# Kernel tuning notes

Measured on AMD Instinct MI355X. Metric: run time of the kernel, lower is better.

Reference implementation:

```python
import jax, jax.numpy as jnp
import numpy as np

B, T, E = 128, 128, 1024
MD = 50          # mask_dim
H = 256          # per-direction GRU hidden (l_hidden_size=512)
D = 512          # biGRU output dim
CO = 256         # conv output channels
K = 4            # CRF tags (2+2)
NL = 3           # sentiment labels
C1, C2 = 0.1, 0.1


def setup_inputs() -> dict:
    key = jax.random.key(0)
    ks = jax.random.split(key, 16)
    IN = E + MD
    g = lambda k, s, sc=0.05: jax.random.normal(k, s, dtype=jnp.float32) * sc
    z = lambda s: jnp.zeros(s, jnp.float32)
    return {
        "sents": jax.random.normal(ks[0], (B, T, E), dtype=jnp.float32),
        "masks": jax.random.randint(ks[1], (B, T), 0, 2),
        "labels": jax.random.randint(ks[2], (B,), 0, NL),
        "lens": jnp.maximum(jax.random.randint(ks[3], (B,), 1, T + 1), 1),
        "mask_emb": g(ks[4], (2, MD), 1.0),
        "Wih_f": g(ks[5], (3 * H, IN)), "Whh_f": g(ks[6], (3 * H, H)),
        "bih_f": z((3 * H,)), "bhh_f": z((3 * H,)),
        "Wih_b": g(ks[7], (3 * H, IN)), "Whh_b": g(ks[8], (3 * H, H)),
        "bih_b": z((3 * H,)), "bhh_b": z((3 * H,)),
        "conv_w": g(ks[9], (CO, D, 3)), "conv_b": z((CO,)),
        "W_tri": g(ks[10], (K, CO)), "b_tri": z((K,)),
        "transitions": g(ks[11], (K, K), 1.0),
        "W_lab": g(ks[12], (NL, CO)), "b_lab": z((NL,)),
    }


def _gru(xg, mask, Whh, bhh, reverse):
    # xg: [T,B,3H] precomputed input projections; mask: [T,B,1]
    Hh = Whh.shape[1]

    def step(h, inp):
        gg, m = inp
        hg = h @ Whh.T + bhh
        r = jax.nn.sigmoid(gg[:, :Hh] + hg[:, :Hh])
        zt = jax.nn.sigmoid(gg[:, Hh:2 * Hh] + hg[:, Hh:2 * Hh])
        n = jnp.tanh(gg[:, 2 * Hh:] + r * hg[:, 2 * Hh:])
        hn = (1.0 - zt) * n + zt * h
        hn = m * hn + (1.0 - m) * h  # padded steps carry state (packed-seq semantics)
        return hn, hn

    h0 = jnp.zeros((xg.shape[1], Hh), xg.dtype)
    _, hs = jax.lax.scan(step, h0, (xg, mask), reverse=reverse)
    return hs  # [T,B,H]


def reference(sents, masks, labels, lens, mask_emb, Wih_f, Whh_f, bih_f, bhh_f,
              Wih_b, Whh_b, bih_b, bhh_b, conv_w, conv_b, W_tri, b_tri,
              transitions, W_lab, b_lab):
    wm = (jnp.arange(T)[None, :] < lens[:, None]).astype(jnp.float32)  # [B,T]
    # SimpleCatTgtMasked: concat mask embedding
    x = jnp.concatenate([sents, mask_emb[masks]], axis=-1)  # [B,T,E+MD]
    mT = wm.T[:, :, None]  # [T,B,1]
    xg_f = jnp.einsum('btc,gc->tbg', x, Wih_f) + bih_f
    xg_b = jnp.einsum('btc,gc->tbg', x, Wih_b) + bih_b
    hf = _gru(xg_f, mT, Whh_f, bhh_f, False)
    hb = _gru(xg_b, mT, Whh_b, bhh_b, True)
    ctx = jnp.concatenate([hf, hb], axis=-1).transpose(1, 0, 2)  # [B,T,D]
    # Conv1d(D->CO, k=3, pad=1) + ReLU
    c = jax.lax.conv_general_dilated(ctx.transpose(0, 2, 1), conv_w, (1,), ((1, 1),),
                                     dimension_numbers=('NCH', 'OIH', 'NCH'))
    ctx2 = jax.nn.relu(c + conv_b[None, :, None]).transpose(0, 2, 1)  # [B,T,CO]
    feats = jnp.einsum('btc,kc->btk', ctx2, W_tri) + b_tri  # [B,T,K]
    # masked linear-chain CRF forward-backward (log-space)
    fT = feats.transpose(1, 0, 2)  # [T,B,K]
    mS = wm.T[1:, :, None]         # [T-1,B,1]

    def fstep(a, inp):
        f_t, m_t = inp
        an = f_t + jax.nn.logsumexp(a[:, :, None] + transitions[None], axis=1)
        a = m_t * an + (1.0 - m_t) * a
        return a, a

    a0 = fT[0]
    _, alphas = jax.lax.scan(fstep, a0, (fT[1:], mS))
    alpha = jnp.concatenate([a0[None], alphas], axis=0)  # [T,B,K]

    def bstep(b, inp):
        f_n, m_n = inp  # feats/mask at t+1
        bn = jax.nn.logsumexp(transitions[None] + (f_n + b)[:, None, :], axis=2)
        b = m_n * bn + (1.0 - m_n) * b
        return b, b

    b_last = jnp.zeros_like(a0)
    _, betas = jax.lax.scan(bstep, b_last, (fT[1:], mS), reverse=True)
    beta = jnp.concatenate([betas, b_last[None]], axis=0)  # [T,B,K]

    marg = jax.nn.softmax(alpha + beta, axis=-1)  # [T,B,K], = exp(alpha+beta-logZ)
    sp = marg[:, :, 1].T * wm  # [B,T] select polarity, zero past length
    gamma = sp.sum(axis=1) / 2.0
    sent_v = jnp.einsum('bt,btc->bc', sp, ctx2) / gamma[:, None]  # [B,CO]
    scores = sent_v @ W_lab.T + b_lab  # [B,NL]
    logp = jax.nn.log_softmax(scores, axis=1)
    cls_loss = -jnp.mean(logp[jnp.arange(B), labels])
    pena = jax.nn.relu(transitions[1, 0] - transitions[0, 0]) + \
           jax.nn.relu(transitions[0, 1] - transitions[1, 1])
    s_prob_norm = jnp.mean(sp.sum(axis=1))
    norm_pen = C1 * pena + C2 * s_prob_norm
    return jnp.stack([cls_loss, norm_pen])
```

## Files before the change

kernel.cpp:

```cpp
#include <hip/hip_runtime.h>
#include <hip/hip_bf16.h>
#include <math.h>

#define B_ 128
#define T_ 128
#define E_ 1024
#define IN_ 1074
#define H_ 256
#define G3_ 768
#define D_ 512
#define CO_ 256

typedef unsigned int uint_t;
typedef _Float16 v2h __attribute__((ext_vector_type(2)));
typedef _Float16 f16x8 __attribute__((ext_vector_type(8)));
typedef float f32x4 __attribute__((ext_vector_type(4)));


__global__ void k_prep_me(const float* __restrict__ mask_emb,
                          const float* __restrict__ Wf, const float* __restrict__ bf,
                          const float* __restrict__ Wb, const float* __restrict__ bb,
                          float* __restrict__ me) {
    int idx = blockIdx.x * 256 + threadIdx.x;
    if (idx >= 2 * 2 * G3_) return;
    int dir = idx / (2 * G3_);
    int rem = idx % (2 * G3_);
    int m = rem / G3_;
    int g = rem % G3_;
    const float* W = dir ? Wb : Wf;
    const float* bi = dir ? bb : bf;
    float acc = bi[g];
    const float* wrow = W + (size_t)g * IN_ + E_;
    const float* e = mask_emb + m * 50;
    #pragma unroll 10
    for (int c = 0; c < 50; ++c) acc += e[c] * wrow[c];
    me[idx] = acc;
}

__device__ __forceinline__ uint_t pk2(float a, float b) {
    uint_t u0 = (uint_t)__builtin_bit_cast(unsigned short, (_Float16)a);
    uint_t u1 = (uint_t)__builtin_bit_cast(unsigned short, (_Float16)b);
    return u0 | (u1 << 16);
}

__global__ void k_prep_wh(const float* __restrict__ Wf, const float* __restrict__ Wb,
                          uint_t* __restrict__ wq) {
    int idx = blockIdx.x * 256 + threadIdx.x;
    if (idx >= 196608) return;
    int u = idx & 3;
    int j = (idx >> 2) & 255;
    int rest = idx >> 10;
    int p = rest % 3;
    int dq = rest / 3;
    int q = dq & 31;
    int d = dq >> 5;
    int g = p * 256 + j;
    int kp = 4 * q + u;
    const float* W = d ? Wb : Wf;
    float w0 = W[(size_t)g * H_ + 2 * kp];
    float w1 = W[(size_t)g * H_ + 2 * kp + 1];
    wq[idx] = pk2(w0, w1);
}

__global__ void k_prep_w2(const float* __restrict__ cw, unsigned short* __restrict__ W2) {
    int i = blockIdx.x * 256 + threadIdx.x;
    if (i >= CO_ * 1536) return;
    int co = i / 1536;
    int k = i % 1536;
    int j = k >> 9;
    int d = k & 511;
    float v = cw[(size_t)co * (D_ * 3) + d * 3 + j];
    W2[i] = __builtin_bit_cast(unsigned short, (_Float16)v);
}

__global__ __launch_bounds__(256) void k_cvt_sents(const float* __restrict__ in,
                                                   uint_t* __restrict__ out) {
    int i = blockIdx.x * 256 + threadIdx.x;
    float4 a = reinterpret_cast<const float4*>(in)[i * 2];
    float4 b = reinterpret_cast<const float4*>(in)[i * 2 + 1];
    uint4 o;
    o.x = pk2(a.x, a.y); o.y = pk2(a.z, a.w);
    o.z = pk2(b.x, b.y); o.w = pk2(b.z, b.w);
    reinterpret_cast<uint4*>(out)[i] = o;
}

__global__ __launch_bounds__(256) void k_cvt_w(const float* __restrict__ Wf,
                                               const float* __restrict__ Wb,
                                               uint_t* __restrict__ out) {
    int i = blockIdx.x * 256 + threadIdx.x;
    if (i >= 1536 * 128) return;
    int n = i >> 7, kq = i & 127;
    int dir = n >= G3_;
    int g = n - dir * G3_;
    const float* src = (dir ? Wb : Wf) + (size_t)g * IN_ + kq * 8;
    float2 a = reinterpret_cast<const float2*>(src)[0];
    float2 b = reinterpret_cast<const float2*>(src)[1];
    float2 c = reinterpret_cast<const float2*>(src)[2];
    float2 d = reinterpret_cast<const float2*>(src)[3];
    uint4 o;
    o.x = pk2(a.x, a.y); o.y = pk2(b.x, b.y);
    o.z = pk2(c.x, c.y); o.w = pk2(d.x, d.y);
    reinterpret_cast<uint4*>(out)[i] = o;
}


__device__ __forceinline__ void gload16(const void* g, void* l) {
    __builtin_amdgcn_global_load_lds(
        (const __attribute__((address_space(1))) void*)g,
        (__attribute__((address_space(3))) void*)l, 16, 0, 0);
}

__global__ __launch_bounds__(256) void k_gemm_mfma(
        const _Float16* __restrict__ A16, const _Float16* __restrict__ W16,
        const float* __restrict__ me, const int* __restrict__ masks,
        float* __restrict__ xgf, float* __restrict__ xgb) {
    __shared__ _Float16 As[4096];
    __shared__ _Float16 Bs[4096];
    const int bid = blockIdx.x;
    const int logical = (bid & 7) * 192 + (bid >> 3);
    const int mt = logical / 12, nt = logical % 12;
    const int bm = mt * 128, bn = nt * 128;
    const int tid = threadIdx.x;
    const int w = tid >> 6, lane = tid & 63;
    const int wr = w >> 1, wc = w & 1;

    const int rl = lane & 15;
    const int kb = (lane >> 4) * 16;
    const int st0 = w, st1 = 4 + w;
    const char* gA0 = (const char*)A16 + (size_t)(bm + st0 * 16 + rl) * 2048 + kb;
    const char* gA1 = (const char*)A16 + (size_t)(bm + st1 * 16 + rl) * 2048 + kb;
    const char* gB0 = (const char*)W16 + (size_t)(bn + st0 * 16 + rl) * 2048 + kb;
    const char* gB1 = (const char*)W16 + (size_t)(bn + st1 * 16 + rl) * 2048 + kb;
    char* lA0 = (char*)As + w * 1024;
    char* lA1 = (char*)As + 4096 + w * 1024;
    char* lB0 = (char*)Bs + w * 1024;
    char* lB1 = (char*)Bs + 4096 + w * 1024;

    f32x4 acc[4][4];
    #pragma unroll
    for (int m = 0; m < 4; ++m)
        #pragma unroll
        for (int n = 0; n < 4; ++n)
            acc[m][n] = (f32x4){0.f, 0.f, 0.f, 0.f};

    for (int kB = 0; kB < 2048; kB += 64) {
        gload16(gA0 + kB, lA0);
        gload16(gA1 + kB, lA1);
        gload16(gB0 + kB, lB0);
        gload16(gB1 + kB, lB1);
        __syncthreads();
        f16x8 af[4], bf[4];
        #pragma unroll
        for (int m = 0; m < 4; ++m)
            af[m] = *reinterpret_cast<const f16x8*>(
                (const char*)As + (wr * 4 + m) * 1024 + lane * 16);
        #pragma unroll
        for (int n = 0; n < 4; ++n)
            bf[n] = *reinterpret_cast<const f16x8*>(
                (const char*)Bs + (wc * 4 + n) * 1024 + lane * 16);
        #pragma unroll
        for (int m = 0; m < 4; ++m)
            #pragma unroll
            for (int n = 0; n < 4; ++n)
                acc[m][n] = __builtin_amdgcn_mfma_f32_16x16x32_f16(
                    af[m], bf[n], acc[m][n], 0, 0, 0);
        __syncthreads();
    }

    const int qr = (lane >> 4) * 4;
    const int cc = lane & 15;
    #pragma unroll
    for (int m = 0; m < 4; ++m) {
        #pragma unroll
        for (int q = 0; q < 4; ++q) {
            const int bt = bm + wr * 64 + m * 16 + qr + q;
            const int mk = masks[bt];
            const int b = bt >> 7, t = bt & 127;
            #pragma unroll
            for (int n = 0; n < 4; ++n) {
                const int col = bn + wc * 64 + n * 16 + cc;
                const int dir = col >= G3_;
                const int g = col - dir * G3_;
                float v = acc[m][n][q] + me[dir * (2 * G3_) + mk * G3_ + g];
                float* dst = (dir ? xgb : xgf) + ((size_t)(t * B_ + b)) * G3_ + g;
                *dst = v;
            }
        }
    }
}

__device__ __forceinline__ float dot2(uint_t w, uint_t h, float acc) {
#if __has_builtin(__builtin_amdgcn_fdot2)
    return __builtin_amdgcn_fdot2(__builtin_bit_cast(v2h, w),
                                  __builtin_bit_cast(v2h, h), acc, false);
#else
    v2h a = __builtin_bit_cast(v2h, w), b = __builtin_bit_cast(v2h, h);
    return acc + (float)a[0] * (float)b[0] + (float)a[1] * (float)b[1];
#endif
}

__global__ __launch_bounds__(512, 2) void k_gru(
        const float* __restrict__ xgf, const float* __restrict__ xgb,
        const uint_t* __restrict__ wq,
        const float* __restrict__ bhhf, const float* __restrict__ bhhb,
        const int* __restrict__ lens, _Float16* __restrict__ ctx16p) {
    const int dir = blockIdx.y;
    const int b = blockIdx.x;
    const int tid = threadIdx.x;
    const int j = tid & 255;
    const int half = tid >> 8;
    const float* xg = dir ? xgb : xgf;
    const float* bhh = dir ? bhhb : bhhf;
    const uint4* wq4 = (const uint4*)wq + (size_t)dir * (32 * 3 * 256);
    _Float16* c16 = ctx16p + (size_t)b * (T_ + 2) * D_;

    __shared__ uint4 hs4[32];
    __shared__ float part[3][256];
    _Float16* hsf = (_Float16*)hs4;

    c16[tid] = (_Float16)0.f;
    c16[(size_t)(T_ + 1) * D_ + tid] = (_Float16)0.f;

    uint4 w4[3][16];
    #pragma unroll
    for (int c = 0; c < 16; ++c) {
        const int q = half * 16 + c;
        #pragma unroll
        for (int p = 0; p < 3; ++p)
            w4[p][c] = wq4[((size_t)q * 3 + p) * 256 + j];
    }

    if (tid < 32) hs4[tid] = (uint4){0u, 0u, 0u, 0u};
    const int len = lens[b];
    const float bh0 = bhh[j], bh1 = bhh[H_ + j], bh2 = bhh[2 * H_ + j];
    float hcur = 0.f;
    float g0 = 0.f, g1 = 0.f, g2 = 0.f;
    int t = dir ? (T_ - 1) : 0;
    if (half == 0) {
        const float* r = xg + ((size_t)(t * B_ + b)) * G3_;
        g0 = r[j]; g1 = r[H_ + j]; g2 = r[2 * H_ + j];
    }
    __syncthreads();

    for (int s = 0; s < T_; ++s) {
        const int tn = dir ? (T_ - 2 - s) : (s + 1);
        float n0 = 0.f, n1 = 0.f, n2 = 0.f;
        if (half == 0 && s < T_ - 1) {
            const float* r = xg + ((size_t)(tn * B_ + b)) * G3_;
            n0 = r[j]; n1 = r[H_ + j]; n2 = r[2 * H_ + j];
        }
        float a0 = 0.f, a1 = 0.f, a2 = 0.f;
        #pragma unroll
        for (int c = 0; c < 16; ++c) {
            uint4 hp = hs4[half * 16 + c];
            a0 = dot2(w4[0][c].x, hp.x, a0); a0 = dot2(w4[0][c].y, hp.y, a0);
            a0 = dot2(w4[0][c].z, hp.z, a0); a0 = dot2(w4[0][c].w, hp.w, a0);
            a1 = dot2(w4[1][c].x, hp.x, a1); a1 = dot2(w4[1][c].y, hp.y, a1);
            a1 = dot2(w4[1][c].z, hp.z, a1); a1 = dot2(w4[1][c].w, hp.w, a1);
            a2 = dot2(w4[2][c].x, hp.x, a2); a2 = dot2(w4[2][c].y, hp.y, a2);
            a2 = dot2(w4[2][c].z, hp.z, a2); a2 = dot2(w4[2][c].w, hp.w, a2);
        }
        if (half == 1) {
            part[0][j] = a0; part[1][j] = a1; part[2][j] = a2;
        }
        __syncthreads();
        if (half == 0) {
            a0 += part[0][j]; a1 += part[1][j]; a2 += part[2][j];
            float rg = 1.f / (1.f + expf(-(g0 + a0 + bh0)));
            float zg = 1.f / (1.f + expf(-(g1 + a1 + bh1)));
            float ng = tanhf(g2 + rg * (a2 + bh2));
            float v = (1.f - zg) * ng + zg * hcur;
            hcur = (t < len) ? v : hcur;
            _Float16 h16 = (_Float16)hcur;
            c16[(size_t)(t + 1) * D_ + dir * H_ + j] = h16;
            hsf[j] = h16;
        }
        __syncthreads();
        g0 = n0; g1 = n1; g2 = n2;
        t = tn;
    }
}

__global__ __launch_bounds__(256) void k_conv_mfma(
        const _Float16* __restrict__ C16, const _Float16* __restrict__ W2,
        const float* __restrict__ cb, float* __restrict__ ctx2) {
    __shared__ _Float16 As[4096];
    __shared__ _Float16 Bs[4096];
    const int b = blockIdx.x >> 1;
    const int nt = blockIdx.x & 1;
    const int bn = nt * 128;
    const int tid = threadIdx.x;
    const int w = tid >> 6, lane = tid & 63;
    const int wr = w >> 1, wc = w & 1;
    const int rl = lane & 15;
    const int kb = (lane >> 4) * 16;
    const char* gA0 = (const char*)C16 + ((size_t)(b * (T_ + 2) + w * 16 + rl)) * 1024 + kb;
    const char* gA1 = (const char*)C16 + ((size_t)(b * (T_ + 2) + 64 + w * 16 + rl)) * 1024 + kb;
    const char* gB0 = (const char*)W2 + (size_t)(bn + w * 16 + rl) * 3072 + kb;
    const char* gB1 = (const char*)W2 + (size_t)(bn + 64 + w * 16 + rl) * 3072 + kb;
    char* lA0 = (char*)As + w * 1024;
    char* lA1 = (char*)As + 4096 + w * 1024;
    char* lB0 = (char*)Bs + w * 1024;
    char* lB1 = (char*)Bs + 4096 + w * 1024;

    f32x4 acc[4][4];
    #pragma unroll
    for (int m = 0; m < 4; ++m)
        #pragma unroll
        for (int n = 0; n < 4; ++n)
            acc[m][n] = (f32x4){0.f, 0.f, 0.f, 0.f};

    for (int kB = 0; kB < 3072; kB += 64) {
        gload16(gA0 + kB, lA0);
        gload16(gA1 + kB, lA1);
        gload16(gB0 + kB, lB0);
        gload16(gB1 + kB, lB1);
        __syncthreads();
        f16x8 af[4], bf[4];
        #pragma unroll
        for (int m = 0; m < 4; ++m)
            af[m] = *reinterpret_cast<const f16x8*>(
                (const char*)As + (wr * 4 + m) * 1024 + lane * 16);
        #pragma unroll
        for (int n = 0; n < 4; ++n)
            bf[n] = *reinterpret_cast<const f16x8*>(
                (const char*)Bs + (wc * 4 + n) * 1024 + lane * 16);
        #pragma unroll
        for (int m = 0; m < 4; ++m)
            #pragma unroll
            for (int n = 0; n < 4; ++n)
                acc[m][n] = __builtin_amdgcn_mfma_f32_16x16x32_f16(
                    af[m], bf[n], acc[m][n], 0, 0, 0);
        __syncthreads();
    }

    const int qr = (lane >> 4) * 4;
    const int cc = lane & 15;
    #pragma unroll
    for (int m = 0; m < 4; ++m) {
        #pragma unroll
        for (int q = 0; q < 4; ++q) {
            const int t = wr * 64 + m * 16 + qr + q;
            #pragma unroll
            for (int n = 0; n < 4; ++n) {
                const int co = bn + wc * 64 + n * 16 + cc;
                float v = acc[m][n][q] + cb[co];
                ctx2[((size_t)(b * T_ + t)) * CO_ + co] = fmaxf(v, 0.f);
            }
        }
    }
}

__global__ __launch_bounds__(256) void k_head(
        const float* __restrict__ ctx2, const float* __restrict__ W_tri,
        const float* __restrict__ b_tri, const float* __restrict__ trans,
        const float* __restrict__ W_lab, const float* __restrict__ b_lab,
        const int* __restrict__ lens, const int* __restrict__ labels,
        float* __restrict__ loss_b, float* __restrict__ spsum_b) {
    const int b = blockIdx.x;
    const int tid = threadIdx.x;
    const int w = tid >> 6, lane = tid & 63;
    __shared__ float f_s[T_][4];
    __shared__ float al[T_][4];
    __shared__ float be[T_][4];
    __shared__ float sp_s[T_];
    __shared__ float sv_s[CO_];
    __shared__ float sred[4];
    __shared__ float s_spsum;
    const int len = lens[b];
    const float* base = ctx2 + (size_t)b * T_ * CO_;

    {
        float wt[4][4];
        #pragma unroll
        for (int k = 0; k < 4; ++k)
            #pragma unroll
            for (int q = 0; q < 4; ++q)
                wt[k][q] = W_tri[k * CO_ + lane + 64 * q];
        float bt0 = b_tri[0], bt1 = b_tri[1], bt2 = b_tri[2], bt3 = b_tri[3];
        for (int t = w; t < T_; t += 4) {
            const float* row = base + (size_t)t * CO_;
            float v0 = row[lane], v1 = row[lane + 64],
                  v2 = row[lane + 128], v3 = row[lane + 192];
            float p0 = v0 * wt[0][0] + v1 * wt[0][1] + v2 * wt[0][2] + v3 * wt[0][3];
            float p1 = v0 * wt[1][0] + v1 * wt[1][1] + v2 * wt[1][2] + v3 * wt[1][3];
            float p2 = v0 * wt[2][0] + v1 * wt[2][1] + v2 * wt[2][2] + v3 * wt[2][3];
            float p3 = v0 * wt[3][0] + v1 * wt[3][1] + v2 * wt[3][2] + v3 * wt[3][3];
            #pragma unroll
            for (int off = 32; off > 0; off >>= 1) {
                p0 += __shfl_xor(p0, off);
                p1 += __shfl_xor(p1, off);
                p2 += __shfl_xor(p2, off);
                p3 += __shfl_xor(p3, off);
            }
            if (lane == 0) {
                f_s[t][0] = p0 + bt0; f_s[t][1] = p1 + bt1;
                f_s[t][2] = p2 + bt2; f_s[t][3] = p3 + bt3;
            }
        }
    }
    __syncthreads();

    if (w == 0 && lane < 4) {
        const int j = lane;
        float tc0 = trans[0 * 4 + j], tc1 = trans[1 * 4 + j],
              tc2 = trans[2 * 4 + j], tc3 = trans[3 * 4 + j];
        float a = f_s[0][j];
        al[0][j] = a;
        for (int t = 1; t < T_; ++t) {
            float a0 = __shfl(a, 0), a1 = __shfl(a, 1),
                  a2 = __shfl(a, 2), a3 = __shfl(a, 3);
            float s0 = a0 + tc0, s1 = a1 + tc1, s2 = a2 + tc2, s3 = a3 + tc3;
            float m = fmaxf(fmaxf(s0, s1), fmaxf(s2, s3));
            float sum = expf(s0 - m) + expf(s1 - m) + expf(s2 - m) + expf(s3 - m);
            float an = f_s[t][j] + m + logf(sum);
            if (t < len) a = an;
            al[t][j] = a;
        }
    } else if (w == 1 && lane < 4) {
        const int i = lane;
        float tr0 = trans[i * 4 + 0], tr1 = trans[i * 4 + 1],
              tr2 = trans[i * 4 + 2], tr3 = trans[i * 4 + 3];
        float bb = 0.f;
        be[T_ - 1][i] = 0.f;
        for (int t = T_ - 2; t >= 0; --t) {
            float b0 = __shfl(bb, 0), b1 = __shfl(bb, 1),
                  b2 = __shfl(bb, 2), b3 = __shfl(bb, 3);
            float s0 = tr0 + f_s[t + 1][0] + b0;
            float s1 = tr1 + f_s[t + 1][1] + b1;
            float s2 = tr2 + f_s[t + 1][2] + b2;
            float s3 = tr3 + f_s[t + 1][3] + b3;
            float m = fmaxf(fmaxf(s0, s1), fmaxf(s2, s3));
            float sum = expf(s0 - m) + expf(s1 - m) + expf(s2 - m) + expf(s3 - m);
            float bn = m + logf(sum);
            if (t + 1 < len) bb = bn;
            be[t][i] = bb;
        }
    }
    __syncthreads();

    if (tid < T_) {
        int t = tid;
        float s0 = al[t][0] + be[t][0];
        float s1 = al[t][1] + be[t][1];
        float s2 = al[t][2] + be[t][2];
        float s3 = al[t][3] + be[t][3];
        float m = fmaxf(fmaxf(s0, s1), fmaxf(s2, s3));
        float e0 = expf(s0 - m), e1 = expf(s1 - m), e2 = expf(s2 - m), e3 = expf(s3 - m);
        float p1 = e1 / (e0 + e1 + e2 + e3);
        sp_s[t] = (t < len) ? p1 : 0.f;
    }
    __syncthreads();
    if (w == 0) {
        float s = sp_s[lane] + sp_s[lane + 64];
        #pragma unroll
        for (int off = 32; off > 0; off >>= 1) s += __shfl_xor(s, off);
        if (lane == 0) s_spsum = s;
    }
    __syncthreads();
    const float spsum = s_spsum;

    {
        float acc0 = 0.f, acc1 = 0.f, acc2 = 0.f, acc3 = 0.f;
        #pragma unroll 2
        for (int t = 0; t < T_; t += 4) {
            acc0 += sp_s[t + 0] * base[(size_t)(t + 0) * CO_ + tid];
            acc1 += sp_s[t + 1] * base[(size_t)(t + 1) * CO_ + tid];
            acc2 += sp_s[t + 2] * base[(size_t)(t + 2) * CO_ + tid];
            acc3 += sp_s[t + 3] * base[(size_t)(t + 3) * CO_ + tid];
        }
        sv_s[tid] = (acc0 + acc1 + acc2 + acc3) * 2.f / spsum;
    }
    __syncthreads();

    if (w < 3) {
        const float* wl = W_lab + w * CO_;
        float p = sv_s[lane] * wl[lane] + sv_s[lane + 64] * wl[lane + 64]
                + sv_s[lane + 128] * wl[lane + 128] + sv_s[lane + 192] * wl[lane + 192];
        #pragma unroll
        for (int off = 32; off > 0; off >>= 1) p += __shfl_xor(p, off);
        if (lane == 0) sred[w] = p + b_lab[w];
    }
    __syncthreads();
    if (tid == 0) {
        float m = fmaxf(sred[0], fmaxf(sred[1], sred[2]));
        float lse = m + logf(expf(sred[0] - m) + expf(sred[1] - m) + expf(sred[2] - m));
        loss_b[b] = lse - sred[labels[b]];
        spsum_b[b] = spsum;
    }
}

__global__ void k_final(const float* __restrict__ loss_b, const float* __restrict__ spsum_b,
                        const float* __restrict__ trans, float* __restrict__ out) {
    __shared__ float s1[128], s2[128];
    int tid = threadIdx.x;
    s1[tid] = loss_b[tid];
    s2[tid] = spsum_b[tid];
    __syncthreads();
    for (int off = 64; off > 0; off >>= 1) {
        if (tid < off) { s1[tid] += s1[tid + off]; s2[tid] += s2[tid + off]; }
        __syncthreads();
    }
    if (tid == 0) {
        float pena = fmaxf(trans[1 * 4 + 0] - trans[0 * 4 + 0], 0.f)
                   + fmaxf(trans[0 * 4 + 1] - trans[1 * 4 + 1], 0.f);
        out[0] = s1[0] / (float)B_;
        out[1] = 0.1f * pena + 0.1f * (s2[0] / (float)B_);
    }
}

extern "C" void kernel_launch(void* const* d_in, const int* in_sizes, int n_in,
                              void* d_out, int out_size, void* d_ws, size_t ws_size,
                              hipStream_t stream) {
    const float* sents   = (const float*)d_in[0];
    const int*   masks   = (const int*)d_in[1];
    const int*   labels  = (const int*)d_in[2];
    const int*   lens    = (const int*)d_in[3];
    const float* mask_emb= (const float*)d_in[4];
    const float* Wih_f   = (const float*)d_in[5];
    const float* Whh_f   = (const float*)d_in[6];
    const float* bih_f   = (const float*)d_in[7];
    const float* bhh_f   = (const float*)d_in[8];
    const float* Wih_b   = (const float*)d_in[9];
    const float* Whh_b   = (const float*)d_in[10];
    const float* bih_b   = (const float*)d_in[11];
    const float* bhh_b   = (const float*)d_in[12];
    const float* conv_w  = (const float*)d_in[13];
    const float* conv_b  = (const float*)d_in[14];
    const float* W_tri   = (const float*)d_in[15];
    const float* b_tri   = (const float*)d_in[16];
    const float* trans   = (const float*)d_in[17];
    const float* W_lab   = (const float*)d_in[18];
    const float* b_lab   = (const float*)d_in[19];
    float* out = (float*)d_out;
    float* ws = (float*)d_ws;

    const size_t o_xgf  = 0;
    const size_t o_xgb  = o_xgf  + (size_t)B_ * T_ * G3_;
    const size_t o_ctx  = o_xgb  + (size_t)B_ * T_ * G3_;
    const size_t o_ctx2 = o_ctx  + (size_t)B_ * T_ * D_;
    const size_t o_wp   = o_ctx2 + (size_t)B_ * T_ * CO_;
    const size_t o_me   = o_wp   + (size_t)2 * 32 * 3 * 256 * 4;
    const size_t o_w2   = o_me   + 2 * 2 * G3_;
    const size_t o_lossb= o_w2   + (size_t)D_ * 3 * CO_;
    const size_t o_spsum= o_lossb + B_;

    float* xgf  = ws + o_xgf;
    float* xgb  = ws + o_xgb;
    float* ctx  = ws + o_ctx;
    float* ctx2 = ws + o_ctx2;
    uint_t* wq  = (uint_t*)(ws + o_wp);
    float* me   = ws + o_me;
    unsigned short* W2 = (unsigned short*)(ws + o_w2);
    float* lossb = ws + o_lossb;
    float* spsumb = ws + o_spsum;

    _Float16* sents16 = (_Float16*)ctx;
    _Float16* ctx16p = (_Float16*)ctx;
    _Float16* W16 = (_Float16*)ctx2;

    k_prep_me<<<12, 256, 0, stream>>>(mask_emb, Wih_f, bih_f, Wih_b, bih_b, me);
    k_prep_wh<<<768, 256, 0, stream>>>(Whh_f, Whh_b, wq);
    k_prep_w2<<<1536, 256, 0, stream>>>(conv_w, W2);
    k_cvt_sents<<<8192, 256, 0, stream>>>(sents, (uint_t*)sents16);
    k_cvt_w<<<768, 256, 0, stream>>>(Wih_f, Wih_b, (uint_t*)W16);
    k_gemm_mfma<<<1536, 256, 0, stream>>>(sents16, W16, me, masks, xgf, xgb);
    k_gru<<<dim3(B_, 2), 512, 0, stream>>>(xgf, xgb, wq, bhh_f, bhh_b, lens, ctx16p);
    k_conv_mfma<<<256, 256, 0, stream>>>(ctx16p, (const _Float16*)W2, conv_b, ctx2);
    k_head<<<128, 256, 0, stream>>>(ctx2, W_tri, b_tri, trans, W_lab, b_lab,
                                    lens, labels, lossb, spsumb);
    k_final<<<1, 128, 0, stream>>>(lossb, spsumb, trans, out);
}
```

Baseline: 418.3 us.

## Split GRU recurrent matvec by gate across three thread groups

The GRU recurrence kernel moves from 512 threads, each splitting the hidden dimension in halves across all three gates, to 768 threads where each 256-thread group computes one full gate over the whole hidden vector. This removes the per-thread three-gate accumulation chains, shortens the per-step dependency chain of dot products, and keeps 32 uint4 weight registers per thread pinned with an empty asm. It costs more threads per block, and with launch bounds of 768 threads and 3 blocks per unit it risks register pressure or spilling. The combine step now reads two partial gates from shared memory instead of three.

```diff
diff --git a/kernel.cpp b/kernel.cpp
--- a/kernel.cpp
+++ b/kernel.cpp
@@ -199,7 +199,7 @@
 #endif
 }
 
-__global__ __launch_bounds__(512, 2) void k_gru(
+__global__ __launch_bounds__(768, 3) void k_gru(
         const float* __restrict__ xgf, const float* __restrict__ xgb,
         const uint_t* __restrict__ wq,
         const float* __restrict__ bhhf, const float* __restrict__ bhhb,
@@ -208,35 +208,38 @@
     const int b = blockIdx.x;
     const int tid = threadIdx.x;
     const int j = tid & 255;
-    const int half = tid >> 8;
+    const int p = tid >> 8;
     const float* xg = dir ? xgb : xgf;
     const float* bhh = dir ? bhhb : bhhf;
     const uint4* wq4 = (const uint4*)wq + (size_t)dir * (32 * 3 * 256);
     _Float16* c16 = ctx16p + (size_t)b * (T_ + 2) * D_;
 
     __shared__ uint4 hs4[32];
-    __shared__ float part[3][256];
+    __shared__ float part[2][256];
     _Float16* hsf = (_Float16*)hs4;
 
-    c16[tid] = (_Float16)0.f;
-    c16[(size_t)(T_ + 1) * D_ + tid] = (_Float16)0.f;
-
-    uint4 w4[3][16];
+    if (tid < 512) {
+        c16[tid] = (_Float16)0.f;
+        c16[(size_t)(T_ + 1) * D_ + tid] = (_Float16)0.f;
+    }
+
+    uint4 w4[32];
     #pragma unroll
-    for (int c = 0; c < 16; ++c) {
-        const int q = half * 16 + c;
-        #pragma unroll
-        for (int p = 0; p < 3; ++p)
-            w4[p][c] = wq4[((size_t)q * 3 + p) * 256 + j];
-    }
+    for (int c = 0; c < 32; ++c)
+        w4[c] = wq4[((size_t)c * 3 + p) * 256 + j];
+    #pragma unroll
+    for (int c = 0; c < 32; ++c)
+        asm volatile("" : "+v"(w4[c].x), "+v"(w4[c].y),
+                          "+v"(w4[c].z), "+v"(w4[c].w));
 
     if (tid < 32) hs4[tid] = (uint4){0u, 0u, 0u, 0u};
     const int len = lens[b];
-    const float bh0 = bhh[j], bh1 = bhh[H_ + j], bh2 = bhh[2 * H_ + j];
+    const float bh = bhh[p * H_ + j];
+    const float bh2o = bhh[2 * H_ + j];
     float hcur = 0.f;
     float g0 = 0.f, g1 = 0.f, g2 = 0.f;
     int t = dir ? (T_ - 1) : 0;
-    if (half == 0) {
+    if (p == 0) {
         const float* r = xg + ((size_t)(t * B_ + b)) * G3_;
         g0 = r[j]; g1 = r[H_ + j]; g2 = r[2 * H_ + j];
     }
@@ -245,30 +248,26 @@
     for (int s = 0; s < T_; ++s) {
         const int tn = dir ? (T_ - 2 - s) : (s + 1);
         float n0 = 0.f, n1 = 0.f, n2 = 0.f;
-        if (half == 0 && s < T_ - 1) {
+        if (p == 0 && s < T_ - 1) {
             const float* r = xg + ((size_t)(tn * B_ + b)) * G3_;
             n0 = r[j]; n1 = r[H_ + j]; n2 = r[2 * H_ + j];
         }
-        float a0 = 0.f, a1 = 0.f, a2 = 0.f;
-        #pragma unroll
-        for (int c = 0; c < 16; ++c) {
-            uint4 hp = hs4[half * 16 + c];
-            a0 = dot2(w4[0][c].x, hp.x, a0); a0 = dot2(w4[0][c].y, hp.y, a0);
-            a0 = dot2(w4[0][c].z, hp.z, a0); a0 = dot2(w4[0][c].w, hp.w, a0);
-            a1 = dot2(w4[1][c].x, hp.x, a1); a1 = dot2(w4[1][c].y, hp.y, a1);
-            a1 = dot2(w4[1][c].z, hp.z, a1); a1 = dot2(w4[1][c].w, hp.w, a1);
-            a2 = dot2(w4[2][c].x, hp.x, a2); a2 = dot2(w4[2][c].y, hp.y, a2);
-            a2 = dot2(w4[2][c].z, hp.z, a2); a2 = dot2(w4[2][c].w, hp.w, a2);
-        }
-        if (half == 1) {
-            part[0][j] = a0; part[1][j] = a1; part[2][j] = a2;
-        }
-        __syncthreads();
-        if (half == 0) {
-            a0 += part[0][j]; a1 += part[1][j]; a2 += part[2][j];
-            float rg = 1.f / (1.f + expf(-(g0 + a0 + bh0)));
-            float zg = 1.f / (1.f + expf(-(g1 + a1 + bh1)));
-            float ng = tanhf(g2 + rg * (a2 + bh2));
+        float a = 0.f;
+        #pragma unroll
+        for (int c = 0; c < 32; ++c) {
+            uint4 hp = hs4[c];
+            a = dot2(w4[c].x, hp.x, a);
+            a = dot2(w4[c].y, hp.y, a);
+            a = dot2(w4[c].z, hp.z, a);
+            a = dot2(w4[c].w, hp.w, a);
+        }
+        if (p > 0) part[p - 1][j] = a;
+        __syncthreads();
+        if (p == 0) {
+            float a0 = a, a1 = part[0][j], a2 = part[1][j];
+            float rg = 1.f / (1.f + expf(-(g0 + a0 + bh)));
+            float zg = 1.f / (1.f + expf(-(g1 + a1 + bhh[H_ + j])));
+            float ng = tanhf(g2 + rg * (a2 + bh2o));
             float v = (1.f - zg) * ng + zg * hcur;
             hcur = (t < len) ? v : hcur;
             _Float16 h16 = (_Float16)hcur;
@@ -565,7 +564,7 @@
     k_cvt_sents<<<8192, 256, 0, stream>>>(sents, (uint_t*)sents16);
     k_cvt_w<<<768, 256, 0, stream>>>(Wih_f, Wih_b, (uint_t*)W16);
     k_gemm_mfma<<<1536, 256, 0, stream>>>(sents16, W16, me, masks, xgf, xgb);
-    k_gru<<<dim3(B_, 2), 512, 0, stream>>>(xgf, xgb, wq, bhh_f, bhh_b, lens, ctx16p);
+    k_gru<<<dim3(B_, 2), 768, 0, stream>>>(xgf, xgb, wq, bhh_f, bhh_b, lens, ctx16p);
     k_conv_mfma<<<256, 256, 0, stream>>>(ctx16p, (const _Float16*)W2, conv_b, ctx2);
     k_head<<<128, 256, 0, stream>>>(ctx2, W_tri, b_tri, trans, W_lab, b_lab,
                                     lens, labels, lossb, spsumb);
```

After: 439.0 us. 1.05x slower.

## Quantize GRU recurrent weights and hidden state to int8 with sdot4

Applied to the files above, without the earlier changes.

Replaces the fp16 fdot2 recurrent matvec in the GRU with int8 per-row-scaled weights and an int8-quantized hidden state (scale 127), accumulated in integers via sdot4 and dequantized before the gates. Two new prep kernels compute per-row max-abs scales and pack the weights. The aim is to halve weight register footprint and dot-product instruction count in the serial recurrence, at the cost of much coarser numerical precision in the recurrent path, which may break accuracy tolerance.

```diff
diff --git a/kernel.cpp b/kernel.cpp
--- a/kernel.cpp
+++ b/kernel.cpp
@@ -43,23 +43,44 @@
     return u0 | (u1 << 16);
 }
 
-__global__ void k_prep_wh(const float* __restrict__ Wf, const float* __restrict__ Wb,
-                          uint_t* __restrict__ wq) {
-    int idx = blockIdx.x * 256 + threadIdx.x;
-    if (idx >= 196608) return;
-    int u = idx & 3;
-    int j = (idx >> 2) & 255;
-    int rest = idx >> 10;
+__global__ void k_scale(const float* __restrict__ Wf, const float* __restrict__ Wb,
+                        float* __restrict__ dq, float* __restrict__ inv) {
+    int r = blockIdx.x * 256 + threadIdx.x;
+    if (r >= 1536) return;
+    int d = r / G3_;
+    int g = r % G3_;
+    const float* W = (d ? Wb : Wf) + (size_t)g * H_;
+    float m = 0.f;
+    for (int k = 0; k < H_; ++k) m = fmaxf(m, fabsf(W[k]));
+    dq[r] = m / 16129.f;
+    inv[r] = (m > 0.f) ? 127.f / m : 0.f;
+}
+
+__global__ void k_quant(const float* __restrict__ Wf, const float* __restrict__ Wb,
+                        const float* __restrict__ inv, uint_t* __restrict__ wi8) {
+    int i = blockIdx.x * 256 + threadIdx.x;
+    if (i >= 98304) return;
+    int w = i & 3;
+    int j = (i >> 2) & 255;
+    int rest = i >> 10;
     int p = rest % 3;
-    int dq = rest / 3;
-    int q = dq & 31;
-    int d = dq >> 5;
+    int rest2 = rest / 3;
+    int q16 = rest2 & 7;
+    int khd = rest2 >> 3;
+    int kh = khd & 1;
+    int d = khd >> 1;
     int g = p * 256 + j;
-    int kp = 4 * q + u;
-    const float* W = d ? Wb : Wf;
-    float w0 = W[(size_t)g * H_ + 2 * kp];
-    float w1 = W[(size_t)g * H_ + 2 * kp + 1];
-    wq[idx] = pk2(w0, w1);
+    int k0 = kh * 128 + q16 * 16 + w * 4;
+    const float* W = (d ? Wb : Wf) + (size_t)g * H_ + k0;
+    float iv = inv[d * G3_ + g];
+    uint_t u = 0;
+    #pragma unroll
+    for (int c = 0; c < 4; ++c) {
+        int q = __float2int_rn(W[c] * iv);
+        q = max(-127, min(127, q));
+        u |= ((uint_t)(q & 0xff)) << (8 * c);
+    }
+    wi8[i] = u;
 }
 
 __global__ void k_prep_w2(const float* __restrict__ cw, unsigned short* __restrict__ W2) {
@@ -189,54 +210,57 @@
     }
 }
 
-__device__ __forceinline__ float dot2(uint_t w, uint_t h, float acc) {
-#if __has_builtin(__builtin_amdgcn_fdot2)
-    return __builtin_amdgcn_fdot2(__builtin_bit_cast(v2h, w),
-                                  __builtin_bit_cast(v2h, h), acc, false);
+__device__ __forceinline__ int sdot4(uint_t a, uint_t b, int c) {
+#if __has_builtin(__builtin_amdgcn_sdot4)
+    return __builtin_amdgcn_sdot4((int)a, (int)b, c, false);
 #else
-    v2h a = __builtin_bit_cast(v2h, w), b = __builtin_bit_cast(v2h, h);
-    return acc + (float)a[0] * (float)b[0] + (float)a[1] * (float)b[1];
+    int r = c;
+    r += ((int)(a << 24) >> 24) * ((int)(b << 24) >> 24);
+    r += ((int)(a << 16) >> 24) * ((int)(b << 16) >> 24);
+    r += ((int)(a << 8) >> 24) * ((int)(b << 8) >> 24);
+    r += ((int)a >> 24) * ((int)b >> 24);
+    return r;
 #endif
 }
 
 __global__ __launch_bounds__(512, 2) void k_gru(
         const float* __restrict__ xgf, const float* __restrict__ xgb,
-        const uint_t* __restrict__ wq,
+        const uint_t* __restrict__ wi8, const float* __restrict__ dq,
         const float* __restrict__ bhhf, const float* __restrict__ bhhb,
         const int* __restrict__ lens, _Float16* __restrict__ ctx16p) {
     const int dir = blockIdx.y;
     const int b = blockIdx.x;
     const int tid = threadIdx.x;
     const int j = tid & 255;
-    const int half = tid >> 8;
+    const int kh = tid >> 8;
     const float* xg = dir ? xgb : xgf;
     const float* bhh = dir ? bhhb : bhhf;
-    const uint4* wq4 = (const uint4*)wq + (size_t)dir * (32 * 3 * 256);
+    const uint4* wp4 = (const uint4*)wi8 + (size_t)dir * (2 * 8 * 3 * 256);
     _Float16* c16 = ctx16p + (size_t)b * (T_ + 2) * D_;
 
-    __shared__ uint4 hs4[32];
-    __shared__ float part[3][256];
-    _Float16* hsf = (_Float16*)hs4;
+    __shared__ uint_t hq_s[64];
+    __shared__ int part[3][256];
 
     c16[tid] = (_Float16)0.f;
     c16[(size_t)(T_ + 1) * D_ + tid] = (_Float16)0.f;
 
-    uint4 w4[3][16];
+    uint4 w4[3][8];
     #pragma unroll
-    for (int c = 0; c < 16; ++c) {
-        const int q = half * 16 + c;
+    for (int q = 0; q < 8; ++q)
         #pragma unroll
         for (int p = 0; p < 3; ++p)
-            w4[p][c] = wq4[((size_t)q * 3 + p) * 256 + j];
-    }
-
-    if (tid < 32) hs4[tid] = (uint4){0u, 0u, 0u, 0u};
+            w4[p][q] = wp4[((size_t)((kh * 8 + q) * 3 + p)) * 256 + j];
+
+    if (tid < 64) hq_s[tid] = 0u;
     const int len = lens[b];
+    const float dq0 = dq[dir * G3_ + j];
+    const float dq1 = dq[dir * G3_ + 256 + j];
+    const float dq2 = dq[dir * G3_ + 512 + j];
     const float bh0 = bhh[j], bh1 = bhh[H_ + j], bh2 = bhh[2 * H_ + j];
     float hcur = 0.f;
     float g0 = 0.f, g1 = 0.f, g2 = 0.f;
     int t = dir ? (T_ - 1) : 0;
-    if (half == 0) {
+    if (kh == 0) {
         const float* r = xg + ((size_t)(t * B_ + b)) * G3_;
         g0 = r[j]; g1 = r[H_ + j]; g2 = r[2 * H_ + j];
     }
@@ -245,35 +269,38 @@
     for (int s = 0; s < T_; ++s) {
         const int tn = dir ? (T_ - 2 - s) : (s + 1);
         float n0 = 0.f, n1 = 0.f, n2 = 0.f;
-        if (half == 0 && s < T_ - 1) {
+        if (kh == 0 && s < T_ - 1) {
             const float* r = xg + ((size_t)(tn * B_ + b)) * G3_;
             n0 = r[j]; n1 = r[H_ + j]; n2 = r[2 * H_ + j];
         }
-        float a0 = 0.f, a1 = 0.f, a2 = 0.f;
-        #pragma unroll
-        for (int c = 0; c < 16; ++c) {
-            uint4 hp = hs4[half * 16 + c];
-            a0 = dot2(w4[0][c].x, hp.x, a0); a0 = dot2(w4[0][c].y, hp.y, a0);
-            a0 = dot2(w4[0][c].z, hp.z, a0); a0 = dot2(w4[0][c].w, hp.w, a0);
-            a1 = dot2(w4[1][c].x, hp.x, a1); a1 = dot2(w4[1][c].y, hp.y, a1);
-            a1 = dot2(w4[1][c].z, hp.z, a1); a1 = dot2(w4[1][c].w, hp.w, a1);
-            a2 = dot2(w4[2][c].x, hp.x, a2); a2 = dot2(w4[2][c].y, hp.y, a2);
-            a2 = dot2(w4[2][c].z, hp.z, a2); a2 = dot2(w4[2][c].w, hp.w, a2);
-        }
-        if (half == 1) {
+        int a0 = 0, a1 = 0, a2 = 0;
+        const uint4* hv = (const uint4*)hq_s + kh * 8;
+        #pragma unroll
+        for (int q = 0; q < 8; ++q) {
+            uint4 h4 = hv[q];
+            a0 = sdot4(w4[0][q].x, h4.x, a0); a0 = sdot4(w4[0][q].y, h4.y, a0);
+            a0 = sdot4(w4[0][q].z, h4.z, a0); a0 = sdot4(w4[0][q].w, h4.w, a0);
+            a1 = sdot4(w4[1][q].x, h4.x, a1); a1 = sdot4(w4[1][q].y, h4.y, a1);
+            a1 = sdot4(w4[1][q].z, h4.z, a1); a1 = sdot4(w4[1][q].w, h4.w, a1);
+            a2 = sdot4(w4[2][q].x, h4.x, a2); a2 = sdot4(w4[2][q].y, h4.y, a2);
+            a2 = sdot4(w4[2][q].z, h4.z, a2); a2 = sdot4(w4[2][q].w, h4.w, a2);
+        }
+        if (kh == 1) {
             part[0][j] = a0; part[1][j] = a1; part[2][j] = a2;
         }
         __syncthreads();
-        if (half == 0) {
-            a0 += part[0][j]; a1 += part[1][j]; a2 += part[2][j];
-            float rg = 1.f / (1.f + expf(-(g0 + a0 + bh0)));
-            float zg = 1.f / (1.f + expf(-(g1 + a1 + bh1)));
-            float ng = tanhf(g2 + rg * (a2 + bh2));
+        if (kh == 0) {
+            float A0 = (float)(a0 + part[0][j]) * dq0;
+            float A1 = (float)(a1 + part[1][j]) * dq1;
+            float A2 = (float)(a2 + part[2][j]) * dq2;
+            float rg = 1.f / (1.f + expf(-(g0 + A0 + bh0)));
+            float zg = 1.f / (1.f + expf(-(g1 + A1 + bh1)));
+            float ng = tanhf(g2 + rg * (A2 + bh2));
             float v = (1.f - zg) * ng + zg * hcur;
             hcur = (t < len) ? v : hcur;
-            _Float16 h16 = (_Float16)hcur;
-            c16[(size_t)(t + 1) * D_ + dir * H_ + j] = h16;
-            hsf[j] = h16;
+            c16[(size_t)(t + 1) * D_ + dir * H_ + j] = (_Float16)hcur;
+            int qi = __float2int_rn(hcur * 127.f);
+            ((signed char*)hq_s)[j] = (signed char)qi;
         }
         __syncthreads();
         g0 = n0; g1 = n1; g2 = n2;
@@ -549,7 +576,9 @@
     float* xgb  = ws + o_xgb;
     float* ctx  = ws + o_ctx;
     float* ctx2 = ws + o_ctx2;
-    uint_t* wq  = (uint_t*)(ws + o_wp);
+    uint_t* wi8 = (uint_t*)(ws + o_wp);
+    float* dq   = ws + o_wp + 98304;
+    float* invs = ws + o_wp + 98304 + 1536;
     float* me   = ws + o_me;
     unsigned short* W2 = (unsigned short*)(ws + o_w2);
     float* lossb = ws + o_lossb;
@@ -560,12 +589,13 @@
     _Float16* W16 = (_Float16*)ctx2;
 
     k_prep_me<<<12, 256, 0, stream>>>(mask_emb, Wih_f, bih_f, Wih_b, bih_b, me);
-    k_prep_wh<<<768, 256, 0, stream>>>(Whh_f, Whh_b, wq);
+    k_scale<<<6, 256, 0, stream>>>(Whh_f, Whh_b, dq, invs);
+    k_quant<<<384, 256, 0, stream>>>(Whh_f, Whh_b, invs, wi8);
     k_prep_w2<<<1536, 256, 0, stream>>>(conv_w, W2);
     k_cvt_sents<<<8192, 256, 0, stream>>>(sents, (uint_t*)sents16);
     k_cvt_w<<<768, 256, 0, stream>>>(Wih_f, Wih_b, (uint_t*)W16);
     k_gemm_mfma<<<1536, 256, 0, stream>>>(sents16, W16, me, masks, xgf, xgb);
-    k_gru<<<dim3(B_, 2), 512, 0, stream>>>(xgf, xgb, wq, bhh_f, bhh_b, lens, ctx16p);
+    k_gru<<<dim3(B_, 2), 512, 0, stream>>>(xgf, xgb, wi8, dq, bhh_f, bhh_b, lens, ctx16p);
     k_conv_mfma<<<256, 256, 0, stream>>>(ctx16p, (const _Float16*)W2, conv_b, ctx2);
     k_head<<<128, 256, 0, stream>>>(ctx2, W_tri, b_tri, trans, W_lab, b_lab,
                                     lens, labels, lossb, spsumb);
```

Result: faster. 391.7 us (-6.4%).
